# Kernel optimization log

Measured on AMD Instinct MI355X. Metric: run time of the kernel, lower is better.

## Reference

```python
import jax, jax.numpy as jnp
import numpy as np

STATE = 1024

def setup_inputs() -> dict:
    key = jax.random.key(0)
    k1, k2, k3, k4, k5 = jax.random.split(key, 5)
    B, IN, S = 4096, 1024, STATE
    stdv = 1.0 / np.sqrt(S)
    return {
        "input": jax.random.normal(k1, (B, IN), jnp.float32),
        "old_h": jax.random.normal(k2, (B, S), jnp.float32),
        "old_cell": jax.random.normal(k3, (B, S), jnp.float32),
        "weights": jax.random.uniform(k4, (4 * S, IN + S), jnp.float32, -stdv, stdv),
        "bias": jax.random.uniform(k5, (4 * S,), jnp.float32, -stdv, stdv),
    }

def reference(input, old_h, old_cell, weights, bias):
    # Fused gate GEMM: X = [input, old_h] -> [B, IN+S]; gates -> [B, 4S]
    X = jnp.concatenate([input, old_h], axis=1)
    gates = X @ weights.T + bias
    f, i, o, g = jnp.split(gates, 4, axis=1)
    f = jax.nn.sigmoid(f)
    i = jax.nn.sigmoid(i)
    o = jax.nn.sigmoid(o)
    g = jnp.tanh(g)
    new_cell = f * old_cell + i * g
    new_h = o * jnp.tanh(new_cell)
    return new_h, new_cell
```

## Files before the change

kernel.cpp:

```cpp
#include <hip/hip_runtime.h>
#include <stdint.h>

#define NB   4096
#define KD   2048
#define ND   4096
#define SD   1024

#define BM   256
#define BN   256
#define BK   64
#define NKT  (KD / BK)

using f32x4  = __attribute__((ext_vector_type(4))) float;
using bf16x8 = __attribute__((ext_vector_type(8))) short;

typedef const __attribute__((address_space(1))) uint32_t* gas_u32;
typedef __attribute__((address_space(3))) uint32_t* las_u32;

__device__ __forceinline__ unsigned short f2bf(float f) {
    union { float f; uint32_t u; } c; c.f = f;
    uint32_t u = c.u;
    uint32_t r = (u + 0x7fffu + ((u >> 16) & 1u)) >> 16;
    return (unsigned short)r;
}

__device__ __forceinline__ void async_load16(const void* gsrc, void* ldst) {
    __builtin_amdgcn_global_load_lds((gas_u32)gsrc, (las_u32)ldst, 16, 0, 0);
}

__device__ __forceinline__ float frcp(float x) { return __builtin_amdgcn_rcpf(x); }
__device__ __forceinline__ float sigm(float x) { return frcp(1.f + __expf(-x)); }
__device__ __forceinline__ float tanh_fast(float x) {
    return 1.f - 2.f * frcp(1.f + __expf(2.f * x));
}

__global__ void pack_kernel(const float* __restrict__ input,
                            const float* __restrict__ old_h,
                            const float* __restrict__ weights,
                            const float* __restrict__ bias,
                            unsigned short* __restrict__ Xb,
                            unsigned short* __restrict__ Wb,
                            float* __restrict__ biasR) {
    const int XCH = NB * (KD / 4);
    const int WCH = ND * (KD / 4);
    const int BCH = ND / 4;
    const int total = XCH + WCH + BCH;
    for (int c = blockIdx.x * blockDim.x + threadIdx.x; c < total;
         c += gridDim.x * blockDim.x) {
        if (c < XCH) {
            int b  = c >> 9;
            int k  = (c & 511) << 2;
            const float* src = (k < 1024) ? (input + (size_t)b * 1024 + k)
                                          : (old_h + (size_t)b * 1024 + (k - 1024));
            float4 v = *reinterpret_cast<const float4*>(src);
            ushort4 o;
            o.x = f2bf(v.x); o.y = f2bf(v.y); o.z = f2bf(v.z); o.w = f2bf(v.w);
            *reinterpret_cast<ushort4*>(Xb + (size_t)b * KD + k) = o;
        } else if (c < XCH + WCH) {
            int cc = c - XCH;
            int n  = cc >> 9;
            int k  = (cc & 511) << 2;
            int srow = ((n >> 4) & 3) * SD + ((n >> 6) * 16 + (n & 15));
            float4 v = *reinterpret_cast<const float4*>(weights + (size_t)srow * KD + k);
            ushort4 o;
            o.x = f2bf(v.x); o.y = f2bf(v.y); o.z = f2bf(v.z); o.w = f2bf(v.w);
            *reinterpret_cast<ushort4*>(Wb + (size_t)n * KD + k) = o;
        } else {
            int n4 = (c - XCH - WCH) << 2;
            #pragma unroll
            for (int t = 0; t < 4; ++t) {
                int n = n4 + t;
                biasR[n] = bias[((n >> 4) & 3) * SD + ((n >> 6) * 16 + (n & 15))];
            }
        }
    }
}

#define SEG(DB, AB, HALF) (((((DB) * 2 + (AB)) * 2) + (HALF)) * 8192)

#define SBAR   __builtin_amdgcn_s_barrier()
#define SFENCE __builtin_amdgcn_sched_barrier(0)
#define ASM_VMCNT4 asm volatile("s_waitcnt vmcnt(4)" ::: "memory")

__launch_bounds__(512, 2)
__global__ void lstm_gemm(const unsigned short* __restrict__ Xb,
                          const unsigned short* __restrict__ Wb,
                          const float* __restrict__ biasR,
                          const float* __restrict__ old_cell,
                          float* __restrict__ new_h,
                          float* __restrict__ new_cell) {
    __shared__ unsigned short lds[65536];

    const int tid  = threadIdx.x;
    const int lane = tid & 63;
    const int wid  = tid >> 6;
    const int wm   = wid >> 2;
    const int wn   = wid & 3;
    const int l15  = lane & 15;
    const int krow = lane >> 4;

    const int wg    = blockIdx.x;
    const int swz   = (wg & 7) * 32 + (wg >> 3);
    const int mblk  = swz >> 4;
    const int nblk  = swz & 15;
    const int rbase = mblk * BM;
    const int nbase = nblk * BN;

    const int c0 = tid, c1 = tid + 512;
    const int srow0 = c0 >> 3, sk0 = ((c0 & 7) ^ (srow0 & 7)) * 8;
    const int srow1 = c1 >> 3, sk1 = ((c1 & 7) ^ (srow1 & 7)) * 8;

    f32x4  acc[8][4] = {};
    bf16x8 a[4];
    bf16x8 bk0[4];
    bf16x8 bk1[4];

#define STAGE(PTR, TB, KT, DB, AB, HALF) do {                                   \
        async_load16((PTR) + (size_t)((TB) + (HALF) * 128 + srow0) * KD +       \
                         (KT) * BK + sk0,                                       \
                     lds + SEG(DB, AB, HALF) + c0 * 8);                         \
        async_load16((PTR) + (size_t)((TB) + (HALF) * 128 + srow1) * KD +       \
                         (KT) * BK + sk1,                                       \
                     lds + SEG(DB, AB, HALF) + c1 * 8);                         \
    } while (0)

#define LOAD_A4(DB, MQ, KK) do {                                                \
        const unsigned short* base_ = lds + SEG(DB, 0, 0) + wm * 8192;          \
        _Pragma("unroll") for (int i_ = 0; i_ < 4; ++i_) {                      \
            int r_ = (MQ) * 64 + i_ * 16 + l15;                                 \
            int s_ = (KK) * 4 + krow;                                           \
            a[i_] = *reinterpret_cast<const bf16x8*>(                           \
                base_ + r_ * 64 + ((s_ ^ (r_ & 7)) * 8));                       \
        }                                                                       \
    } while (0)

#define LOAD_B4(DST, DB, KK) do {                                               \
        const unsigned short* base_ = lds + SEG(DB, 1, 0) + (wn >> 1) * 8192;   \
        _Pragma("unroll") for (int j_ = 0; j_ < 4; ++j_) {                      \
            int r_ = (wn & 1) * 64 + j_ * 16 + l15;                             \
            int s_ = (KK) * 4 + krow;                                           \
            DST[j_] = *reinterpret_cast<const bf16x8*>(                         \
                base_ + r_ * 64 + ((s_ ^ (r_ & 7)) * 8));                       \
        }                                                                       \
    } while (0)

#define MMA16(MQ, BB) do {                                                      \
        _Pragma("unroll") for (int i_ = 0; i_ < 4; ++i_)                        \
        _Pragma("unroll") for (int j_ = 0; j_ < 4; ++j_)                        \
            acc[(MQ) * 4 + i_][j_] =                                            \
                __builtin_amdgcn_mfma_f32_16x16x32_bf16(                        \
                    a[i_], BB[j_], acc[(MQ) * 4 + i_][j_], 0, 0, 0);            \
    } while (0)

    STAGE(Wb, nbase, 0, 0, 1, 0);
    STAGE(Wb, nbase, 0, 0, 1, 1);
    STAGE(Xb, rbase, 0, 0, 0, 0);
    STAGE(Xb, rbase, 0, 0, 0, 1);
    STAGE(Wb, nbase, 1, 1, 1, 0);
    STAGE(Wb, nbase, 1, 1, 1, 1);
    ASM_VMCNT4;
    SBAR;
    SFENCE;

#define KBODY(TT, BUF) do {                                                     \
        const int kt1_ = ((TT) + 1) & (NKT - 1);                                \
        const int kt2_ = ((TT) + 2) & (NKT - 1);                                \
                      \
        STAGE(Xb, rbase, kt1_, (BUF) ^ 1, 0, 0);                                \
        LOAD_A4(BUF, 0, 0);                                                     \
        LOAD_B4(bk0, BUF, 0);                                                   \
        MMA16(0, bk0);                                                          \
        SBAR; SFENCE;                                                           \
                      \
        STAGE(Xb, rbase, kt1_, (BUF) ^ 1, 0, 1);                                \
        LOAD_A4(BUF, 0, 1);                                                     \
        LOAD_B4(bk1, BUF, 1);                                                   \
        MMA16(0, bk1);                                                          \
        SBAR; SFENCE;                                                           \
               \
        STAGE(Wb, nbase, kt2_, BUF, 1, 0);                                      \
        LOAD_A4(BUF, 1, 0);                                                     \
        MMA16(1, bk0);                                                          \
        SBAR; SFENCE;                                                           \
              \
        STAGE(Wb, nbase, kt2_, BUF, 1, 1);                                      \
        LOAD_A4(BUF, 1, 1);                                                     \
        MMA16(1, bk1);                                                          \
        ASM_VMCNT4;                                                             \
        SBAR; SFENCE;                                                           \
    } while (0)

    for (int t = 0; t < NKT; t += 2) {
        KBODY(t, 0);
        KBODY(t + 1, 1);
    }

    const int s = (nblk * 4 + wn) * 16 + l15;
    float bg[4];
    #pragma unroll
    for (int jj = 0; jj < 4; ++jj)
        bg[jj] = biasR[nbase + wn * 64 + jj * 16 + l15];

    #pragma unroll
    for (int mi = 0; mi < 8; ++mi) {
        #pragma unroll
        for (int r = 0; r < 4; ++r) {
            const int row = rbase + wm * 128 + mi * 16 + krow * 4 + r;
            float fg = sigm(acc[mi][0][r] + bg[0]);
            float ig = sigm(acc[mi][1][r] + bg[1]);
            float og = sigm(acc[mi][2][r] + bg[2]);
            float gg = tanh_fast(acc[mi][3][r] + bg[3]);
            float oc = old_cell[(size_t)row * SD + s];
            float nc = fmaf(fg, oc, ig * gg);
            float nh = og * tanh_fast(nc);
            new_h[(size_t)row * SD + s]    = nh;
            new_cell[(size_t)row * SD + s] = nc;
        }
    }
}

extern "C" void kernel_launch(void* const* d_in, const int* in_sizes, int n_in,
                              void* d_out, int out_size, void* d_ws, size_t ws_size,
                              hipStream_t stream) {
    const float* input    = (const float*)d_in[0];
    const float* old_h    = (const float*)d_in[1];
    const float* old_cell = (const float*)d_in[2];
    const float* weights  = (const float*)d_in[3];
    const float* bias     = (const float*)d_in[4];

    unsigned short* Xb  = (unsigned short*)d_ws;
    unsigned short* Wb  = (unsigned short*)((char*)d_ws + (size_t)16777216);
    float*          bR  = (float*)((char*)d_ws + (size_t)33554432);

    float* out_h = (float*)d_out;
    float* out_c = out_h + (size_t)NB * SD;

    pack_kernel<<<2048, 256, 0, stream>>>(input, old_h, weights, bias, Xb, Wb, bR);
    lstm_gemm<<<(NB / BM) * (ND / BN), 512, 0, stream>>>(Xb, Wb, bR, old_cell,
                                                         out_h, out_c);
}
```

Baseline: 77.80 us.

## Replace staggered 4-phase K-loop pipeline with simple double-buffer, one barrier per tile

Drops the fine-grained schedule that issued Xb and Wb stages in four sub-phases with a barrier after each, where W was prefetched two tiles ahead. Each K tile now waits on vmcnt(0), takes one barrier, issues every global-to-LDS load for the next tile, then does all LDS reads and MFMAs for the current tile. This cuts barriers from four to one per tile and simplifies the code. In exchange each tile fully drains outstanding loads before starting, so there is less load/compute overlap and prefetch depth drops from two tiles to one.

```diff
diff --git a/kernel.cpp b/kernel.cpp
--- a/kernel.cpp
+++ b/kernel.cpp
@@ -80,7 +80,7 @@
 
 #define SBAR   __builtin_amdgcn_s_barrier()
 #define SFENCE __builtin_amdgcn_sched_barrier(0)
-#define ASM_VMCNT4 asm volatile("s_waitcnt vmcnt(4)" ::: "memory")
+#define ASM_VMCNT0 asm volatile("s_waitcnt vmcnt(0)" ::: "memory")
 
 __launch_bounds__(512, 2)
 __global__ void lstm_gemm(const unsigned short* __restrict__ Xb,
@@ -111,9 +111,8 @@
     const int srow1 = c1 >> 3, sk1 = ((c1 & 7) ^ (srow1 & 7)) * 8;
 
     f32x4  acc[8][4] = {};
-    bf16x8 a[4];
-    bf16x8 bk0[4];
-    bf16x8 bk1[4];
+    bf16x8 a0[4], a1[4];
+    bf16x8 bk0[4], bk1[4];
 
 #define STAGE(PTR, TB, KT, DB, AB, HALF) do {                                   \
         async_load16((PTR) + (size_t)((TB) + (HALF) * 128 + srow0) * KD +       \
@@ -124,12 +123,12 @@
                      lds + SEG(DB, AB, HALF) + c1 * 8);                         \
     } while (0)
 
-#define LOAD_A4(DB, MQ, KK) do {                                                \
+#define LOAD_A4(DST, DB, MQ, KK) do {                                           \
         const unsigned short* base_ = lds + SEG(DB, 0, 0) + wm * 8192;          \
         _Pragma("unroll") for (int i_ = 0; i_ < 4; ++i_) {                      \
             int r_ = (MQ) * 64 + i_ * 16 + l15;                                 \
             int s_ = (KK) * 4 + krow;                                           \
-            a[i_] = *reinterpret_cast<const bf16x8*>(                           \
+            DST[i_] = *reinterpret_cast<const bf16x8*>(                         \
                 base_ + r_ * 64 + ((s_ ^ (r_ & 7)) * 8));                       \
         }                                                                       \
     } while (0)
@@ -144,50 +143,38 @@
         }                                                                       \
     } while (0)
 
-#define MMA16(MQ, BB) do {                                                      \
+#define MMA16(MQ, AA, BB) do {                                                  \
         _Pragma("unroll") for (int i_ = 0; i_ < 4; ++i_)                        \
         _Pragma("unroll") for (int j_ = 0; j_ < 4; ++j_)                        \
             acc[(MQ) * 4 + i_][j_] =                                            \
                 __builtin_amdgcn_mfma_f32_16x16x32_bf16(                        \
-                    a[i_], BB[j_], acc[(MQ) * 4 + i_][j_], 0, 0, 0);            \
-    } while (0)
-
+                    AA[i_], BB[j_], acc[(MQ) * 4 + i_][j_], 0, 0, 0);           \
+    } while (0)
+
+    STAGE(Xb, rbase, 0, 0, 0, 0);
+    STAGE(Xb, rbase, 0, 0, 0, 1);
     STAGE(Wb, nbase, 0, 0, 1, 0);
     STAGE(Wb, nbase, 0, 0, 1, 1);
-    STAGE(Xb, rbase, 0, 0, 0, 0);
-    STAGE(Xb, rbase, 0, 0, 0, 1);
-    STAGE(Wb, nbase, 1, 1, 1, 0);
-    STAGE(Wb, nbase, 1, 1, 1, 1);
-    ASM_VMCNT4;
-    SBAR;
-    SFENCE;
 
 #define KBODY(TT, BUF) do {                                                     \
         const int kt1_ = ((TT) + 1) & (NKT - 1);                                \
-        const int kt2_ = ((TT) + 2) & (NKT - 1);                                \
-                      \
+        ASM_VMCNT0;                                   \
+        SBAR;                \
+        SFENCE;                               \
         STAGE(Xb, rbase, kt1_, (BUF) ^ 1, 0, 0);                                \
-        LOAD_A4(BUF, 0, 0);                                                     \
+        STAGE(Xb, rbase, kt1_, (BUF) ^ 1, 0, 1);                                \
+        STAGE(Wb, nbase, kt1_, (BUF) ^ 1, 1, 0);                                \
+        STAGE(Wb, nbase, kt1_, (BUF) ^ 1, 1, 1);                                \
         LOAD_B4(bk0, BUF, 0);                                                   \
-        MMA16(0, bk0);                                                          \
-        SBAR; SFENCE;                                                           \
-                      \
-        STAGE(Xb, rbase, kt1_, (BUF) ^ 1, 0, 1);                                \
-        LOAD_A4(BUF, 0, 1);                                                     \
         LOAD_B4(bk1, BUF, 1);                                                   \
-        MMA16(0, bk1);                                                          \
-        SBAR; SFENCE;                                                           \
-               \
-        STAGE(Wb, nbase, kt2_, BUF, 1, 0);                                      \
-        LOAD_A4(BUF, 1, 0);                                                     \
-        MMA16(1, bk0);                                                          \
-        SBAR; SFENCE;                                                           \
-              \
-        STAGE(Wb, nbase, kt2_, BUF, 1, 1);                                      \
-        LOAD_A4(BUF, 1, 1);                                                     \
-        MMA16(1, bk1);                                                          \
-        ASM_VMCNT4;                                                             \
-        SBAR; SFENCE;                                                           \
+        LOAD_A4(a0, BUF, 0, 0);                                                 \
+        LOAD_A4(a1, BUF, 0, 1);                                                 \
+        MMA16(0, a0, bk0);                                                      \
+        MMA16(0, a1, bk1);                                                      \
+        LOAD_A4(a0, BUF, 1, 0);                                                 \
+        LOAD_A4(a1, BUF, 1, 1);                                                 \
+        MMA16(1, a0, bk0);                                                      \
+        MMA16(1, a1, bk1);                                                      \
     } while (0)
 
     for (int t = 0; t < NKT; t += 2) {
```

Measured after the change: 79.85 us. 1.03x slower.
